# Optimization experiments

Hardware: AMD Instinct MI355X
Metric: run time of the kernel (lower is better)

Reference implementation:

```python
import jax, jax.numpy as jnp
import numpy as np


def _morton_inverse_perm(L: int):
    """Return inv such that out_flat = x[..., inv] reproduces ret[i][j] = x[ij].

    i collects odd bits of ij, j collects even bits (Z-order / Morton decode).
    """
    S = int(np.sqrt(L))
    bit_l = L.bit_length()
    ij = np.arange(L, dtype=np.int64)
    i = np.zeros(L, dtype=np.int64)
    j = np.zeros(L, dtype=np.int64)
    for bit in range(bit_l):
        b = (ij >> bit) & 1
        if bit % 2 == 1:
            i += b << (bit // 2)
        else:
            j += b << (bit // 2)
    flat = i * S + j  # destination flat index for source position ij
    inv = np.empty(L, dtype=np.int64)
    inv[flat] = ij    # inverse permutation: gather form
    return inv, S


def setup_inputs() -> dict:
    key = jax.random.key(0)
    B, C, L = 8, 64, 65536  # 256x256 spatial map flattened in Morton order
    x = jax.random.normal(key, (B, C, L), dtype=jnp.float32)
    return {"x": x}


def reference(x) -> jnp.ndarray:
    B, C, L = x.shape
    inv, S = _morton_inverse_perm(L)  # data-independent, static under jit
    inv = jnp.asarray(inv)
    # single gather replaces the quadruple nested scalar-assignment loop
    out = jnp.take(x, inv, axis=2).reshape(B, C, S, S)
    return out
```

## Files before the change

kernel.cpp:

```cpp
#include <hip/hip_runtime.h>


typedef float f32x4 __attribute__((ext_vector_type(4)));

__device__ __forceinline__ unsigned compact1by1(unsigned x) {
    x &= 0x55555555u;
    x = (x ^ (x >> 1)) & 0x33333333u;
    x = (x ^ (x >> 2)) & 0x0f0f0f0fu;
    x = (x ^ (x >> 4)) & 0x00ff00ffu;
    return x;
}

__global__ __launch_bounds__(256) void Morton_decode_69312182223578_kernel(
        const float* __restrict__ x, float* __restrict__ out) {
    const unsigned b    = blockIdx.x;
    const unsigned bc   = b >> 4;
    const unsigned tile = b & 15u;
    const unsigned ti   = tile >> 2;
    const unsigned tj   = tile & 3u;
    const unsigned tile_morton =
        (tj & 1u) | ((ti & 1u) << 1) | ((tj >> 1) << 2) | ((ti >> 1) << 3);

    const f32x4* __restrict__ src =
        (const f32x4*)(x + (size_t)bc * 65536u + ((size_t)tile_morton << 12));
    const unsigned t = threadIdx.x;

    const f32x4 v0 = src[4u * t + 0u];
    const f32x4 v1 = src[4u * t + 1u];
    const f32x4 v2 = src[4u * t + 2u];
    const f32x4 v3 = src[4u * t + 3u];

    const unsigned Jh = compact1by1(t);
    const unsigned Ih = compact1by1(t >> 1);
    const unsigned i0 = ti * 64u + 4u * Ih;
    const unsigned j0 = tj * 64u + 4u * Jh;

    const f32x4 r0 = {v0.x, v0.y, v1.x, v1.y};
    const f32x4 r1 = {v0.z, v0.w, v1.z, v1.w};
    const f32x4 r2 = {v2.x, v2.y, v3.x, v3.y};
    const f32x4 r3 = {v2.z, v2.w, v3.z, v3.w};

    float* p = out + (size_t)bc * 65536u + (size_t)i0 * 256u + j0;
    __builtin_nontemporal_store(r0, (f32x4*)(p));
    __builtin_nontemporal_store(r1, (f32x4*)(p + 256));
    __builtin_nontemporal_store(r2, (f32x4*)(p + 512));
    __builtin_nontemporal_store(r3, (f32x4*)(p + 768));
}

extern "C" void kernel_launch(void* const* d_in, const int* in_sizes, int n_in,
                              void* d_out, int out_size, void* d_ws, size_t ws_size,
                              hipStream_t stream) {
    const float* x = (const float*)d_in[0];
    float* out = (float*)d_out;
    Morton_decode_69312182223578_kernel<<<8192, 256, 0, stream>>>(x, out);
}
```

Measured before the change: 229.3 us.

## Stage Morton-decoded tiles in LDS to emit full-row coalesced stores

Each block now covers a 32-row by 256-column strip. It loads the four Morton sub-tiles feeding that strip, scatters them into padded shared memory, then writes whole 1 KB output rows with 16-byte nontemporal stores. Previously each thread wrote scattered 16-byte chunks across four rows, which gave poorly coalesced writes. The cost is an LDS round-trip, a block barrier and about 33 KB of shared memory per block, which may lower occupancy. The grid is halved.

```diff
diff --git a/kernel.cpp b/kernel.cpp
--- a/kernel.cpp
+++ b/kernel.cpp
@@ -11,40 +11,57 @@
     return x;
 }
 
+#define LDSW 260u
+
 __global__ __launch_bounds__(256) void Morton_decode_69312182223578_kernel(
         const float* __restrict__ x, float* __restrict__ out) {
-    const unsigned b    = blockIdx.x;
-    const unsigned bc   = b >> 4;
-    const unsigned tile = b & 15u;
-    const unsigned ti   = tile >> 2;
-    const unsigned tj   = tile & 3u;
-    const unsigned tile_morton =
-        (tj & 1u) | ((ti & 1u) << 1) | ((tj >> 1) << 2) | ((ti >> 1) << 3);
+    __shared__ float lds[32u * LDSW];
 
-    const f32x4* __restrict__ src =
-        (const f32x4*)(x + (size_t)bc * 65536u + ((size_t)tile_morton << 12));
+    const unsigned b     = blockIdx.x;
+    const unsigned bc    = b >> 3;
+    const unsigned rem   = b & 7u;
+    const unsigned ti    = rem >> 1;
+    const unsigned ihalf = rem & 1u;
+
     const unsigned t = threadIdx.x;
+    const float* img = x + (size_t)bc * 65536u;
 
-    const f32x4 v0 = src[4u * t + 0u];
-    const f32x4 v1 = src[4u * t + 1u];
-    const f32x4 v2 = src[4u * t + 2u];
-    const f32x4 v3 = src[4u * t + 3u];
+    f32x4 v[4][2];
+#pragma unroll
+    for (unsigned c = 0; c < 4; ++c) {
+        const unsigned tm = (c & 1u) | ((ti & 1u) << 1)
+                          | ((c >> 1) << 2) | ((ti >> 1) << 3);
+        const f32x4* src = (const f32x4*)(img + ((size_t)tm << 12) + (ihalf << 11));
+        v[c][0] = src[2u * t + 0u];
+        v[c][1] = src[2u * t + 1u];
+    }
 
-    const unsigned Jh = compact1by1(t);
-    const unsigned Ih = compact1by1(t >> 1);
-    const unsigned i0 = ti * 64u + 4u * Ih;
-    const unsigned j0 = tj * 64u + 4u * Jh;
+    const unsigned g   = t >> 1;
+    const unsigned bq  = t & 1u;
+    const unsigned Jh  = compact1by1(g);
+    const unsigned Ihp = compact1by1(g >> 1);
+    const unsigned r   = 4u * Ihp + 2u * bq;
 
-    const f32x4 r0 = {v0.x, v0.y, v1.x, v1.y};
-    const f32x4 r1 = {v0.z, v0.w, v1.z, v1.w};
-    const f32x4 r2 = {v2.x, v2.y, v3.x, v3.y};
-    const f32x4 r3 = {v2.z, v2.w, v3.z, v3.w};
+#pragma unroll
+    for (unsigned c = 0; c < 4; ++c) {
+        const unsigned col = c * 64u + 4u * Jh;
+        f32x4 w0 = {v[c][0].x, v[c][0].y, v[c][1].x, v[c][1].y};
+        f32x4 w1 = {v[c][0].z, v[c][0].w, v[c][1].z, v[c][1].w};
+        *(f32x4*)(&lds[r * LDSW + col])        = w0;
+        *(f32x4*)(&lds[(r + 1u) * LDSW + col]) = w1;
+    }
 
-    float* p = out + (size_t)bc * 65536u + (size_t)i0 * 256u + j0;
-    __builtin_nontemporal_store(r0, (f32x4*)(p));
-    __builtin_nontemporal_store(r1, (f32x4*)(p + 256));
-    __builtin_nontemporal_store(r2, (f32x4*)(p + 512));
-    __builtin_nontemporal_store(r3, (f32x4*)(p + 768));
+    __syncthreads();
+
+    float* obase = out + (size_t)bc * 65536u + (size_t)(2u * ti + ihalf) * 8192u;
+    const unsigned w_id  = t >> 6;
+    const unsigned lane4 = (t & 63u) * 4u;
+#pragma unroll
+    for (unsigned s = 0; s < 8; ++s) {
+        const unsigned rr = s * 4u + w_id;
+        f32x4 w = *(const f32x4*)(&lds[rr * LDSW + lane4]);
+        __builtin_nontemporal_store(w, (f32x4*)(obase + rr * 256u + lane4));
+    }
 }
 
 extern "C" void kernel_launch(void* const* d_in, const int* in_sizes, int n_in,
@@ -52,5 +69,5 @@
                               hipStream_t stream) {
     const float* x = (const float*)d_in[0];
     float* out = (float*)d_out;
-    Morton_decode_69312182223578_kernel<<<8192, 256, 0, stream>>>(x, out);
+    Morton_decode_69312182223578_kernel<<<4096, 256, 0, stream>>>(x, out);
 }
```

After: 230.7 us. Within noise of the previous version (+0.6%).

## Process four tiles per block with double-buffered register loads

Applied to the files above, without the earlier changes.

Each block now handles four consecutive 64x64 Morton tiles instead of one and loads the next tile's data into a second register buffer while storing the current one. The grid shrinks from 8192 to 2048 blocks. Stores switch from nontemporal to ordinary stores. The aim is more memory-level parallelism per thread and less block-launch overhead, at the cost of more registers and fewer resident waves across the GPU.

```diff
diff --git a/kernel.cpp b/kernel.cpp
--- a/kernel.cpp
+++ b/kernel.cpp
@@ -13,38 +13,42 @@
 
 __global__ __launch_bounds__(256) void Morton_decode_69312182223578_kernel(
         const float* __restrict__ x, float* __restrict__ out) {
-    const unsigned b    = blockIdx.x;
-    const unsigned bc   = b >> 4;
-    const unsigned tile = b & 15u;
-    const unsigned ti   = tile >> 2;
-    const unsigned tj   = tile & 3u;
-    const unsigned tile_morton =
-        (tj & 1u) | ((ti & 1u) << 1) | ((tj >> 1) << 2) | ((ti >> 1) << 3);
-
-    const f32x4* __restrict__ src =
-        (const f32x4*)(x + (size_t)bc * 65536u + ((size_t)tile_morton << 12));
-    const unsigned t = threadIdx.x;
-
-    const f32x4 v0 = src[4u * t + 0u];
-    const f32x4 v1 = src[4u * t + 1u];
-    const f32x4 v2 = src[4u * t + 2u];
-    const f32x4 v3 = src[4u * t + 3u];
-
+    const unsigned t  = threadIdx.x;
     const unsigned Jh = compact1by1(t);
     const unsigned Ih = compact1by1(t >> 1);
-    const unsigned i0 = ti * 64u + 4u * Ih;
-    const unsigned j0 = tj * 64u + 4u * Jh;
 
-    const f32x4 r0 = {v0.x, v0.y, v1.x, v1.y};
-    const f32x4 r1 = {v0.z, v0.w, v1.z, v1.w};
-    const f32x4 r2 = {v2.x, v2.y, v3.x, v3.y};
-    const f32x4 r3 = {v2.z, v2.w, v3.z, v3.w};
+    const unsigned T0 = blockIdx.x << 2;
+    const unsigned bc = T0 >> 4;
+    float* const oimg = out + (size_t)bc * 65536u;
+    const f32x4* const xv = (const f32x4*)x;
 
-    float* p = out + (size_t)bc * 65536u + (size_t)i0 * 256u + j0;
-    __builtin_nontemporal_store(r0, (f32x4*)(p));
-    __builtin_nontemporal_store(r1, (f32x4*)(p + 256));
-    __builtin_nontemporal_store(r2, (f32x4*)(p + 512));
-    __builtin_nontemporal_store(r3, (f32x4*)(p + 768));
+    f32x4 v[2][4];
+    {
+        const f32x4* s = xv + ((size_t)T0 << 10) + 4u * t;
+        v[0][0] = s[0]; v[0][1] = s[1]; v[0][2] = s[2]; v[0][3] = s[3];
+    }
+
+#pragma unroll
+    for (unsigned k = 0; k < 4; ++k) {
+        const unsigned cur = k & 1u;
+        if (k < 3) {
+            const f32x4* s = xv + ((size_t)(T0 + k + 1u) << 10) + 4u * t;
+            v[cur ^ 1u][0] = s[0]; v[cur ^ 1u][1] = s[1];
+            v[cur ^ 1u][2] = s[2]; v[cur ^ 1u][3] = s[3];
+        }
+
+        const unsigned tm = (T0 + k) & 15u;
+        const unsigned tj = (tm & 1u) | ((tm >> 1) & 2u);
+        const unsigned ti = ((tm >> 1) & 1u) | ((tm >> 2) & 2u);
+        float* p = oimg + (size_t)(ti * 64u + 4u * Ih) * 256u + (tj * 64u + 4u * Jh);
+
+        const f32x4 a0 = v[cur][0], a1 = v[cur][1], a2 = v[cur][2], a3 = v[cur][3];
+        f32x4 r;
+        r = (f32x4){a0.x, a0.y, a1.x, a1.y}; *(f32x4*)(p)       = r;
+        r = (f32x4){a0.z, a0.w, a1.z, a1.w}; *(f32x4*)(p + 256) = r;
+        r = (f32x4){a2.x, a2.y, a3.x, a3.y}; *(f32x4*)(p + 512) = r;
+        r = (f32x4){a2.z, a2.w, a3.z, a3.w}; *(f32x4*)(p + 768) = r;
+    }
 }
 
 extern "C" void kernel_launch(void* const* d_in, const int* in_sizes, int n_in,
@@ -52,5 +56,5 @@
                               hipStream_t stream) {
     const float* x = (const float*)d_in[0];
     float* out = (float*)d_out;
-    Morton_decode_69312182223578_kernel<<<8192, 256, 0, stream>>>(x, out);
+    Morton_decode_69312182223578_kernel<<<2048, 256, 0, stream>>>(x, out);
 }
```

New measurement: 231.4 us. Within noise of the previous version (+0.9%).
